# Optimization experiments

Measured on AMD Instinct MI355X. Metric: run time of the kernel, lower is better.

Reference implementation:

```python
import jax, jax.numpy as jnp
import numpy as np

EPS = 1e-12  # F.normalize default eps


def setup_inputs() -> dict:
    key = jax.random.key(0)
    k1, k2 = jax.random.split(key)
    b, c, angRes, h, w = 4, 64, 5, 64, 64
    d = 64  # dims
    x = jax.random.normal(k1, (b, c, angRes * angRes, h, w), dtype=jnp.float32)
    # 1x1 conv weight [3*dims, channels] (kernel size 1, no bias)
    W = jax.random.normal(k2, (3 * d, c), dtype=jnp.float32) * 0.02
    return {"x": x, "W": W}


def reference(x, W):
    b, c, n, h, w = x.shape
    d = W.shape[0] // 3
    # 1x1 conv over angular (u,v) grid == channel matmul; rearranges are free reindexings
    qkv = jnp.einsum('oc,bcnhw->bonhw', W, x)  # [b, 3d, n, h, w]
    q, k, v = jnp.split(qkv, 3, axis=1)        # each [b, d, n, h, w]

    def flat(t):  # '(b h w) c u v -> b (u v) (c h w)'
        return t.transpose(0, 2, 1, 3, 4).reshape(b, n, d * h * w)

    q, k, v = flat(q), flat(k), flat(v)
    # L2-normalize along the (c h w) feature dim (k was normalized on dim=-2 of its
    # transposed layout, which is this same feature dim)
    q = q / jnp.maximum(jnp.linalg.norm(q, axis=-1, keepdims=True), EPS)
    k = k / jnp.maximum(jnp.linalg.norm(k, axis=-1, keepdims=True), EPS)
    att = jax.nn.softmax(jnp.einsum('bnf,bmf->bnm', q, k), axis=-1)  # [b, n, n], n=25
    out = jnp.einsum('bnm,bmf->bnf', att, v)   # [b, n, d*h*w]
    # 'b (u v) (c h w) -> b c (u v) h w'
    return out.reshape(b, n, d, h, w).transpose(0, 2, 1, 3, 4)
```

## Files before the change

kernel.cpp:

```cpp
#include <hip/hip_runtime.h>

#define B   4
#define C   64
#define D   64
#define NN  25
#define HW  4096
#define F   (D*HW)

#define SW  256
#define PT  128

typedef unsigned short ushort_t;
typedef unsigned int   uint_t;
typedef __attribute__((ext_vector_type(8)))  short  short8;
typedef __attribute__((ext_vector_type(16))) float  floatx16;
typedef __attribute__((ext_vector_type(4)))  float  f32x4;
typedef __attribute__((ext_vector_type(4)))  unsigned short us4;

__device__ ushort_t g_Wthi[128 * C];
__device__ ushort_t g_Wtlo[128 * C];
__device__ ushort_t g_Wvhi[D * C];
__device__ ushort_t g_Wvlo[D * C];

__device__ float g_S[B * NN * NN];
__device__ float g_qq[B * NN];
__device__ float g_kk[B * NN];
__device__ float g_attT[B * NN * NN];

static __device__ __forceinline__ ushort_t f2bf(float f) {
    uint_t u = __float_as_uint(f);
    u += 0x7FFFu + ((u >> 16) & 1u);
    return (ushort_t)(u >> 16);
}
static __device__ __forceinline__ float bf2f(ushort_t h) {
    return __uint_as_float((uint_t)h << 16);
}

static __device__ __forceinline__ int lds_x(int p, int c) {
    return p * 64 + ((((c >> 3) ^ (p & 7)) << 3) | (c & 7));
}

__global__ void k_zero() {
    int i = blockIdx.x * 256 + threadIdx.x;
    if (i < 2500)      g_S[i] = 0.f;
    else if (i < 2600) g_qq[i - 2500] = 0.f;
    else if (i < 2700) g_kk[i - 2600] = 0.f;
}

__global__ void k_wprep(const float* __restrict__ W) {
    int i = blockIdx.x * 256 + threadIdx.x;
    if (i < 128 * 64) {
        float w = W[i];
        ushort_t hi = f2bf(w);
        g_Wthi[i] = hi;
        g_Wtlo[i] = f2bf(w - bf2f(hi));
    } else if (i < 192 * 64) {
        float w = W[i];
        int j = i - 128 * 64;
        ushort_t hi = f2bf(w);
        g_Wvhi[j] = hi;
        g_Wvlo[j] = f2bf(w - bf2f(hi));
    }
}

__global__ void __launch_bounds__(256, 4)
k_proj(const float* __restrict__ x,
       ushort_t* __restrict__ Q, ushort_t* __restrict__ K,
       float* __restrict__ V) {
    __shared__ ushort_t sXhi[PT * 64];
    __shared__ ushort_t sXlo[PT * 64];

    const int t  = threadIdx.x;
    const int wv = t >> 6, ln = t & 63;
    const int n  = blockIdx.y, b = blockIdx.z;
    const int tile = blockIdx.x;
    const int gp0  = tile * PT;

    const int row = ln & 31, kh = (ln >> 5) * 8, d0 = wv * 32;
    short8 ahi[4], alo[4];
#pragma unroll
    for (int ks = 0; ks < 4; ++ks) {
        ahi[ks] = *(const short8*)&g_Wthi[(d0 + row) * 64 + ks * 16 + kh];
        alo[ks] = *(const short8*)&g_Wtlo[(d0 + row) * 64 + ks * 16 + kh];
    }

    {
        const int c16 = wv * 16;
#pragma unroll
        for (int cg = 0; cg < 4; ++cg) {
            const int c4 = c16 + cg * 4;
            const float* xc = x + ((size_t)(b * C + c4) * NN + n) * HW + gp0;
#pragma unroll
            for (int ph = 0; ph < 2; ++ph) {
                const int p = ph * 64 + ln;
                float v[4];
#pragma unroll
                for (int i = 0; i < 4; ++i) v[i] = xc[(size_t)i * NN * HW + p];
                us4 h, l;
#pragma unroll
                for (int i = 0; i < 4; ++i) {
                    ushort_t hi = f2bf(v[i]);
                    h[i] = hi;
                    l[i] = f2bf(v[i] - bf2f(hi));
                }
                *(us4*)&sXhi[lds_x(p, c4)] = h;
                *(us4*)&sXlo[lds_x(p, c4)] = l;
            }
        }
    }
    __syncthreads();

    ushort_t* __restrict__ O = (wv < 2) ? Q : K;
    const int slab = (wv < 2) ? wv : wv - 2;
    const size_t nbase = (size_t)(b * NN + n) * F;

    float nrm = 0.f;
#pragma unroll
    for (int pt = 0; pt < 4; ++pt) {
        const int pcol = pt * 32 + row;
        floatx16 acc;
#pragma unroll
        for (int r = 0; r < 16; ++r) acc[r] = 0.f;
#pragma unroll
        for (int ks = 0; ks < 4; ++ks) {
            const int c0 = ks * 16 + kh;
            short8 bhi = *(const short8*)&sXhi[lds_x(pcol, c0)];
            short8 blo = *(const short8*)&sXlo[lds_x(pcol, c0)];
            acc = __builtin_amdgcn_mfma_f32_32x32x16_bf16(ahi[ks], bhi, acc, 0, 0, 0);
            acc = __builtin_amdgcn_mfma_f32_32x32x16_bf16(alo[ks], bhi, acc, 0, 0, 0);
            acc = __builtin_amdgcn_mfma_f32_32x32x16_bf16(ahi[ks], blo, acc, 0, 0, 0);
        }
#pragma unroll
        for (int r4 = 0; r4 < 4; ++r4) {
            us4 h;
#pragma unroll
            for (int j = 0; j < 4; ++j) {
                const float a = acc[r4 * 4 + j];
                nrm += a * a;
                h[j] = f2bf(a);
            }
            *(us4*)&O[nbase + (((size_t)((tile * 2 + slab) * 16 + pt * 4 + r4)) << 8)
                      + ln * 4] = h;
        }
    }
    for (int off = 32; off > 0; off >>= 1) nrm += __shfl_xor(nrm, off);
    if (ln == 0) atomicAdd(((wv < 2) ? g_qq : g_kk) + b * NN + n, nrm);

    {
        const int sv = wv & 1, ph = wv >> 1;
        short8 vhi[4], vlo[4];
#pragma unroll
        for (int ks = 0; ks < 4; ++ks) {
            vhi[ks] = *(const short8*)&g_Wvhi[(sv * 32 + row) * 64 + ks * 16 + kh];
            vlo[ks] = *(const short8*)&g_Wvlo[(sv * 32 + row) * 64 + ks * 16 + kh];
        }
#pragma unroll
        for (int pt = 0; pt < 2; ++pt) {
            const int pcol = ph * 64 + pt * 32 + row;
            floatx16 acc;
#pragma unroll
            for (int r = 0; r < 16; ++r) acc[r] = 0.f;
#pragma unroll
            for (int ks = 0; ks < 4; ++ks) {
                const int c0 = ks * 16 + kh;
                short8 bhi = *(const short8*)&sXhi[lds_x(pcol, c0)];
                short8 blo = *(const short8*)&sXlo[lds_x(pcol, c0)];
                acc = __builtin_amdgcn_mfma_f32_32x32x16_bf16(vhi[ks], bhi, acc, 0, 0, 0);
                acc = __builtin_amdgcn_mfma_f32_32x32x16_bf16(vlo[ks], bhi, acc, 0, 0, 0);
                acc = __builtin_amdgcn_mfma_f32_32x32x16_bf16(vhi[ks], blo, acc, 0, 0, 0);
            }
#pragma unroll
            for (int r4 = 0; r4 < 4; ++r4) {
                f32x4 o;
#pragma unroll
                for (int j = 0; j < 4; ++j) o[j] = acc[r4 * 4 + j];
                V[nbase + (((size_t)((((tile * 2 + sv) * 2 + ph) * 2 + pt) * 4 + r4)) << 8)
                  + ln * 4] = o[0],
                *(f32x4*)&V[nbase + (((size_t)((((tile * 2 + sv) * 2 + ph) * 2 + pt) * 4
                  + r4)) << 8) + ln * 4] = o;
            }
        }
    }
}

__global__ void k_sqk(const ushort_t* __restrict__ Q, const ushort_t* __restrict__ K) {
    const int t  = threadIdx.x;
    const int wv = t >> 6, ln = t & 63;
    const int b  = blockIdx.y;
    const int row  = ln & 31;
    const int rowc = (row < NN) ? row : (NN - 1);
    const int kh   = (ln >> 5) * 8;
    const size_t f0 = (size_t)blockIdx.x * (4 * SW) + (size_t)wv * SW;
    const ushort_t* Qp = Q + ((size_t)b * NN + rowc) * F + f0 + kh;
    const ushort_t* Kp = K + ((size_t)b * NN + rowc) * F + f0 + kh;

    floatx16 acc;
#pragma unroll
    for (int r = 0; r < 16; ++r) acc[r] = 0.f;

    for (int s = 0; s < SW / 16; ++s) {
        short8 aq = *(const short8*)(Qp + s * 16);
        short8 bk = *(const short8*)(Kp + s * 16);
        acc = __builtin_amdgcn_mfma_f32_32x32x16_bf16(aq, bk, acc, 0, 0, 0);
    }

    __shared__ float redS[4][64][17];
#pragma unroll
    for (int r = 0; r < 16; ++r) redS[wv][ln][r] = acc[r];
    __syncthreads();
    if (wv == 0) {
#pragma unroll
        for (int r = 0; r < 16; ++r) {
            float v = redS[0][ln][r] + redS[1][ln][r] + redS[2][ln][r] + redS[3][ln][r];
            const int srow = (r & 3) + 8 * (r >> 2) + 4 * (ln >> 5);
            const int scol = ln & 31;
            if (srow < NN && scol < NN)
                atomicAdd(&g_S[((size_t)b * NN + srow) * NN + scol], v);
        }
    }
}

__global__ void k_softmax() {
    const int b = blockIdx.x, n = threadIdx.x;
    if (n >= NN) return;
    const float qn = fmaxf(sqrtf(g_qq[b * NN + n]), 1e-12f);
    float l[NN], mx = -1e30f;
#pragma unroll
    for (int m = 0; m < NN; ++m) {
        const float km = fmaxf(sqrtf(g_kk[b * NN + m]), 1e-12f);
        l[m] = g_S[((size_t)b * NN + n) * NN + m] / (qn * km);
        mx = fmaxf(mx, l[m]);
    }
    float s = 0.f;
#pragma unroll
    for (int m = 0; m < NN; ++m) { l[m] = expf(l[m] - mx); s += l[m]; }
    const float inv = 1.f / s;
#pragma unroll
    for (int m = 0; m < NN; ++m) g_attT[((size_t)b * NN + m) * NN + n] = l[m] * inv;
}

__global__ void __launch_bounds__(256, 4)
k_outmix(const float* __restrict__ V, float* __restrict__ out) {
    const int tid = blockIdx.x * 256 + threadIdx.x;
    const int b   = blockIdx.y;
    const float* Vb = V + (size_t)b * NN * F + (size_t)tid * 4;
    const float* at = g_attT + b * NN * NN;

    f32x4 acc[NN];
#pragma unroll
    for (int n = 0; n < NN; ++n) acc[n] = 0.f;
#pragma unroll 5
    for (int m = 0; m < NN; ++m) {
        const f32x4 v = *(const f32x4*)(Vb + (size_t)m * F);
#pragma unroll
        for (int n = 0; n < NN; ++n) acc[n] += at[m * NN + n] * v;
    }

    const int ln = tid & 63, c0 = tid >> 6;
    const int r4 = c0 & 3, pt = (c0 >> 2) & 1, ph = (c0 >> 3) & 1;
    const int sv = (c0 >> 4) & 1, tile = c0 >> 5;
    const int p  = tile * 128 + ph * 64 + pt * 32 + (ln & 31);
    const int db = sv * 32 + 8 * r4 + 4 * (ln >> 5);
#pragma unroll
    for (int n = 0; n < NN; ++n)
#pragma unroll
        for (int j = 0; j < 4; ++j)
            out[((size_t)(b * D + db + j) * NN + n) * HW + p] = acc[n][j];
}

extern "C" void kernel_launch(void* const* d_in, const int* in_sizes, int n_in,
                              void* d_out, int out_size, void* d_ws, size_t ws_size,
                              hipStream_t stream) {
    const float* x = (const float*)d_in[0];
    const float* W = (const float*)d_in[1];
    float* outf = (float*)d_out;

    ushort_t* Q = (ushort_t*)d_out;
    ushort_t* K = Q + (size_t)B * NN * F;
    float*    V = (float*)d_ws;

    k_zero   <<<dim3(11),           256, 0, stream>>>();
    k_wprep  <<<dim3(48),           256, 0, stream>>>(W);
    k_proj   <<<dim3(HW/PT, NN, B), 256, 0, stream>>>(x, Q, K, V);
    k_sqk    <<<dim3(F/(4*SW), B),  256, 0, stream>>>(Q, K);
    k_softmax<<<dim3(B),             64, 0, stream>>>();
    k_outmix <<<dim3(F/1024, B),    256, 0, stream>>>(V, outf);
}
```

Before: 309.7 us.

## Stage Q/K chunks through swizzled LDS in S=QK^T kernel with 512 threads

The Gram-matrix kernel used to load Q and K directly from global memory with short8 per lane, where each lane read a different row (strided, poorly coalesced). It now cooperatively loads 256-element chunks of all 25 rows into XOR-swizzled shared memory with contiguous per-row accesses. Eight waves then each run MFMAs from LDS, and the reduction sums eight partials. A redundant scalar store in the projection kernel is also removed. The cost is extra LDS traffic and barriers, plus a larger reduction per block.

```diff
diff --git a/kernel.cpp b/kernel.cpp
--- a/kernel.cpp
+++ b/kernel.cpp
@@ -7,12 +7,14 @@
 #define HW  4096
 #define F   (D*HW)
 
-#define SW  256
 #define PT  128
+#define QCH 256
+#define NCH 4
 
 typedef unsigned short ushort_t;
 typedef unsigned int   uint_t;
 typedef __attribute__((ext_vector_type(8)))  short  short8;
+typedef __attribute__((ext_vector_type(8)))  unsigned short us8;
 typedef __attribute__((ext_vector_type(16))) float  floatx16;
 typedef __attribute__((ext_vector_type(4)))  float  f32x4;
 typedef __attribute__((ext_vector_type(4)))  unsigned short us4;
@@ -174,44 +176,67 @@
                 f32x4 o;
 #pragma unroll
                 for (int j = 0; j < 4; ++j) o[j] = acc[r4 * 4 + j];
-                V[nbase + (((size_t)((((tile * 2 + sv) * 2 + ph) * 2 + pt) * 4 + r4)) << 8)
-                  + ln * 4] = o[0],
                 *(f32x4*)&V[nbase + (((size_t)((((tile * 2 + sv) * 2 + ph) * 2 + pt) * 4
-                  + r4)) << 8) + ln * 4] = o;
+                    + r4)) << 8) + ln * 4] = o;
             }
         }
     }
 }
 
-__global__ void k_sqk(const ushort_t* __restrict__ Q, const ushort_t* __restrict__ K) {
+__global__ void __launch_bounds__(512, 8)
+k_sqk(const ushort_t* __restrict__ Q, const ushort_t* __restrict__ K) {
+    __shared__ __align__(16) unsigned char smem[35904];
+    ushort_t* sQ = (ushort_t*)smem;
+    ushort_t* sK = (ushort_t*)(smem + 16384);
+    float (*redS)[64][17] = (float (*)[64][17])smem;
+
     const int t  = threadIdx.x;
     const int wv = t >> 6, ln = t & 63;
     const int b  = blockIdx.y;
-    const int row  = ln & 31;
-    const int rowc = (row < NN) ? row : (NN - 1);
-    const int kh   = (ln >> 5) * 8;
-    const size_t f0 = (size_t)blockIdx.x * (4 * SW) + (size_t)wv * SW;
-    const ushort_t* Qp = Q + ((size_t)b * NN + rowc) * F + f0 + kh;
-    const ushort_t* Kp = K + ((size_t)b * NN + rowc) * F + f0 + kh;
+    const size_t fbase = (size_t)blockIdx.x * (QCH * NCH);
+
+    const int col = t & 31;
+    const int r0  = t >> 5;
+    const int rr  = ln & 31;
+    const int khalf = ln >> 5;
 
     floatx16 acc;
 #pragma unroll
     for (int r = 0; r < 16; ++r) acc[r] = 0.f;
 
-    for (int s = 0; s < SW / 16; ++s) {
-        short8 aq = *(const short8*)(Qp + s * 16);
-        short8 bk = *(const short8*)(Kp + s * 16);
-        acc = __builtin_amdgcn_mfma_f32_32x32x16_bf16(aq, bk, acc, 0, 0, 0);
-    }
-
-    __shared__ float redS[4][64][17];
+    for (int ch = 0; ch < NCH; ++ch) {
+        const size_t f0 = fbase + (size_t)ch * QCH;
+        if (ch) __syncthreads();
+#pragma unroll
+        for (int pass = 0; pass < 2; ++pass) {
+            const int r  = pass * 16 + r0;
+            const int rc = (r < NN) ? r : (NN - 1);
+            const size_t g = ((size_t)b * NN + rc) * F + f0 + col * 8;
+            const int lx = r * QCH + ((col ^ (r & 7)) * 8);
+            *(us8*)&sQ[lx] = *(const us8*)(Q + g);
+            *(us8*)&sK[lx] = *(const us8*)(K + g);
+        }
+        __syncthreads();
+#pragma unroll
+        for (int i = 0; i < 2; ++i) {
+            const int cunit = (wv * 2 + i) * 2 + khalf;
+            const int lx = rr * QCH + ((cunit ^ (rr & 7)) * 8);
+            short8 aq = *(const short8*)&sQ[lx];
+            short8 bk = *(const short8*)&sK[lx];
+            acc = __builtin_amdgcn_mfma_f32_32x32x16_bf16(aq, bk, acc, 0, 0, 0);
+        }
+    }
+
+    __syncthreads();
 #pragma unroll
     for (int r = 0; r < 16; ++r) redS[wv][ln][r] = acc[r];
     __syncthreads();
     if (wv == 0) {
 #pragma unroll
         for (int r = 0; r < 16; ++r) {
-            float v = redS[0][ln][r] + redS[1][ln][r] + redS[2][ln][r] + redS[3][ln][r];
+            float v = 0.f;
+#pragma unroll
+            for (int w = 0; w < 8; ++w) v += redS[w][ln][r];
             const int srow = (r & 3) + 8 * (r >> 2) + 4 * (ln >> 5);
             const int scol = ln & 31;
             if (srow < NN && scol < NN)
@@ -279,10 +304,10 @@
     ushort_t* K = Q + (size_t)B * NN * F;
     float*    V = (float*)d_ws;
 
-    k_zero   <<<dim3(11),           256, 0, stream>>>();
-    k_wprep  <<<dim3(48),           256, 0, stream>>>(W);
-    k_proj   <<<dim3(HW/PT, NN, B), 256, 0, stream>>>(x, Q, K, V);
-    k_sqk    <<<dim3(F/(4*SW), B),  256, 0, stream>>>(Q, K);
-    k_softmax<<<dim3(B),             64, 0, stream>>>();
-    k_outmix <<<dim3(F/1024, B),    256, 0, stream>>>(V, outf);
-}
+    k_zero   <<<dim3(11),               256, 0, stream>>>();
+    k_wprep  <<<dim3(48),               256, 0, stream>>>(W);
+    k_proj   <<<dim3(HW/PT, NN, B),     256, 0, stream>>>(x, Q, K, V);
+    k_sqk    <<<dim3(F/(QCH*NCH), B),   512, 0, stream>>>(Q, K);
+    k_softmax<<<dim3(B),                 64, 0, stream>>>();
+    k_outmix <<<dim3(F/1024, B),        256, 0, stream>>>(V, outf);
+}
```

Measured after the change: 302.9 us. 2.2% less time.

## Fuse QKV projection with Q·Kᵀ score computation, keeping Q/K in LDS

Applied to the files above, without the earlier changes.

Merges the projection and score kernels: each 512-thread block handles 32 pixels across all 25 angular views for one 32-channel slab, keeps bf16 Q and K tiles in shared memory, and computes the partial 25x25 score matrix directly from LDS. This removes the global-memory round trip of Q and K and one kernel launch. The x loads are double-buffered in registers and the V output layout and outmix indexing are changed to match. In exchange, each block uses about 100KB of LDS, which limits occupancy, and weights are reloaded per view iteration.

```diff
diff --git a/kernel.cpp b/kernel.cpp
--- a/kernel.cpp
+++ b/kernel.cpp
@@ -7,9 +7,6 @@
 #define HW  4096
 #define F   (D*HW)
 
-#define SW  256
-#define PT  128
-
 typedef unsigned short ushort_t;
 typedef unsigned int   uint_t;
 typedef __attribute__((ext_vector_type(8)))  short  short8;
@@ -34,10 +31,6 @@
 }
 static __device__ __forceinline__ float bf2f(ushort_t h) {
     return __uint_as_float((uint_t)h << 16);
-}
-
-static __device__ __forceinline__ int lds_x(int p, int c) {
-    return p * 64 + ((((c >> 3) ^ (p & 7)) << 3) | (c & 7));
 }
 
 __global__ void k_zero() {
@@ -63,159 +56,141 @@
     }
 }
 
-__global__ void __launch_bounds__(256, 4)
-k_proj(const float* __restrict__ x,
-       ushort_t* __restrict__ Q, ushort_t* __restrict__ K,
-       float* __restrict__ V) {
-    __shared__ ushort_t sXhi[PT * 64];
-    __shared__ ushort_t sXlo[PT * 64];
-
-    const int t  = threadIdx.x;
-    const int wv = t >> 6, ln = t & 63;
-    const int n  = blockIdx.y, b = blockIdx.z;
-    const int tile = blockIdx.x;
-    const int gp0  = tile * PT;
-
-    const int row = ln & 31, kh = (ln >> 5) * 8, d0 = wv * 32;
-    short8 ahi[4], alo[4];
-#pragma unroll
-    for (int ks = 0; ks < 4; ++ks) {
-        ahi[ks] = *(const short8*)&g_Wthi[(d0 + row) * 64 + ks * 16 + kh];
-        alo[ks] = *(const short8*)&g_Wtlo[(d0 + row) * 64 + ks * 16 + kh];
-    }
+__global__ void __launch_bounds__(512, 2)
+k_projS(const float* __restrict__ x, float* __restrict__ V) {
+    __shared__ ushort_t sQ[25 * 1024];
+    __shared__ ushort_t sK[25 * 1024];
+
+    const int t    = threadIdx.x;
+    const int w    = t >> 6, ln = t & 63;
+    const int slab = blockIdx.y, b = blockIdx.z;
+    const int p0   = blockIdx.x * 32;
+    const int row  = ln & 31, kh = ln >> 5, kh8 = kh * 8;
+    const size_t cstride = (size_t)NN * HW;
+    const float* xp = x + ((size_t)(b * C) * NN) * HW + p0 + row;
+
+    float xbufA[32], xbufB[32];
+#pragma unroll
+    for (int ks = 0; ks < 4; ++ks)
+#pragma unroll
+        for (int j = 0; j < 8; ++j)
+            xbufA[ks * 8 + j] =
+                xp[(size_t)(ks * 16 + kh8 + j) * cstride + (size_t)w * HW];
+
+#pragma unroll
+    for (int i = 0; i < 4; ++i) {
+        const int n = w + i * 8;
+        if (n > 24) break;
+        const int n2 = n + 8;
+        float (&cur)[32] = (i & 1) ? xbufB : xbufA;
+        float (&nxt)[32] = (i & 1) ? xbufA : xbufB;
+        if (n2 <= 24) {
+#pragma unroll
+            for (int ks = 0; ks < 4; ++ks)
+#pragma unroll
+                for (int j = 0; j < 8; ++j)
+                    nxt[ks * 8 + j] =
+                        xp[(size_t)(ks * 16 + kh8 + j) * cstride + (size_t)n2 * HW];
+        }
+
+        short8 qhi[4], qlo[4], khi[4], klo[4], vhi[4], vlo[4];
+#pragma unroll
+        for (int ks = 0; ks < 4; ++ks) {
+            const int off = ks * 16 + kh8;
+            qhi[ks] = *(const short8*)&g_Wthi[(slab * 32 + row) * 64 + off];
+            qlo[ks] = *(const short8*)&g_Wtlo[(slab * 32 + row) * 64 + off];
+            khi[ks] = *(const short8*)&g_Wthi[(64 + slab * 32 + row) * 64 + off];
+            klo[ks] = *(const short8*)&g_Wtlo[(64 + slab * 32 + row) * 64 + off];
+            vhi[ks] = *(const short8*)&g_Wvhi[(slab * 32 + row) * 64 + off];
+            vlo[ks] = *(const short8*)&g_Wvlo[(slab * 32 + row) * 64 + off];
+        }
+
+        short8 bhi[4], blo[4];
+#pragma unroll
+        for (int ks = 0; ks < 4; ++ks)
+#pragma unroll
+            for (int j = 0; j < 8; ++j) {
+                const float v = cur[ks * 8 + j];
+                const ushort_t hi = f2bf(v);
+                bhi[ks][j] = (short)hi;
+                blo[ks][j] = (short)f2bf(v - bf2f(hi));
+            }
+
+        floatx16 aQ, aK, aV;
+#pragma unroll
+        for (int r = 0; r < 16; ++r) { aQ[r] = 0.f; aK[r] = 0.f; aV[r] = 0.f; }
+#pragma unroll
+        for (int ks = 0; ks < 4; ++ks) {
+            aQ = __builtin_amdgcn_mfma_f32_32x32x16_bf16(qhi[ks], bhi[ks], aQ, 0, 0, 0);
+            aQ = __builtin_amdgcn_mfma_f32_32x32x16_bf16(qlo[ks], bhi[ks], aQ, 0, 0, 0);
+            aQ = __builtin_amdgcn_mfma_f32_32x32x16_bf16(qhi[ks], blo[ks], aQ, 0, 0, 0);
+            aK = __builtin_amdgcn_mfma_f32_32x32x16_bf16(khi[ks], bhi[ks], aK, 0, 0, 0);
+            aK = __builtin_amdgcn_mfma_f32_32x32x16_bf16(klo[ks], bhi[ks], aK, 0, 0, 0);
+            aK = __builtin_amdgcn_mfma_f32_32x32x16_bf16(khi[ks], blo[ks], aK, 0, 0, 0);
+            aV = __builtin_amdgcn_mfma_f32_32x32x16_bf16(vhi[ks], bhi[ks], aV, 0, 0, 0);
+            aV = __builtin_amdgcn_mfma_f32_32x32x16_bf16(vlo[ks], bhi[ks], aV, 0, 0, 0);
+            aV = __builtin_amdgcn_mfma_f32_32x32x16_bf16(vhi[ks], blo[ks], aV, 0, 0, 0);
+        }
+
+        float nq = 0.f, nk = 0.f;
+#pragma unroll
+        for (int r4 = 0; r4 < 4; ++r4) {
+            us4 hq, hk; f32x4 vv;
+#pragma unroll
+            for (int j = 0; j < 4; ++j) {
+                const float q = aQ[r4 * 4 + j], k = aK[r4 * 4 + j];
+                nq += q * q; nk += k * k;
+                hq[j] = f2bf(q); hk[j] = f2bf(k);
+                vv[j] = aV[r4 * 4 + j];
+            }
+            const int lx = n * 1024 + ((r4 * 32 + (ln >> 1)) ^ (n & 7)) * 8
+                         + (ln & 1) * 4;
+            *(us4*)&sQ[lx] = hq;
+            *(us4*)&sK[lx] = hk;
+            *(f32x4*)&V[((size_t)(b * NN + n)) * F
+                        + (size_t)((blockIdx.x * 2 + slab) * 4 + r4) * 256
+                        + ln * 4] = vv;
+        }
+        for (int off = 32; off > 0; off >>= 1) {
+            nq += __shfl_xor(nq, off);
+            nk += __shfl_xor(nk, off);
+        }
+        if (ln == 0) {
+            atomicAdd(&g_qq[b * NN + n], nq);
+            atomicAdd(&g_kk[b * NN + n], nk);
+        }
+    }
+    __syncthreads();
 
     {
-        const int c16 = wv * 16;
-#pragma unroll
-        for (int cg = 0; cg < 4; ++cg) {
-            const int c4 = c16 + cg * 4;
-            const float* xc = x + ((size_t)(b * C + c4) * NN + n) * HW + gp0;
-#pragma unroll
-            for (int ph = 0; ph < 2; ++ph) {
-                const int p = ph * 64 + ln;
-                float v[4];
-#pragma unroll
-                for (int i = 0; i < 4; ++i) v[i] = xc[(size_t)i * NN * HW + p];
-                us4 h, l;
-#pragma unroll
-                for (int i = 0; i < 4; ++i) {
-                    ushort_t hi = f2bf(v[i]);
-                    h[i] = hi;
-                    l[i] = f2bf(v[i] - bf2f(hi));
-                }
-                *(us4*)&sXhi[lds_x(p, c4)] = h;
-                *(us4*)&sXlo[lds_x(p, c4)] = l;
+        const int rc = (row < NN) ? row : (NN - 1);
+        floatx16 acc;
+#pragma unroll
+        for (int r = 0; r < 16; ++r) acc[r] = 0.f;
+#pragma unroll
+        for (int i = 0; i < 8; ++i) {
+            const int g  = (w * 8 + i) * 2 + kh;
+            const int lx = rc * 1024 + (g ^ (rc & 7)) * 8;
+            short8 aq = *(const short8*)&sQ[lx];
+            short8 bk = *(const short8*)&sK[lx];
+            acc = __builtin_amdgcn_mfma_f32_32x32x16_bf16(aq, bk, acc, 0, 0, 0);
+        }
+        __syncthreads();
+        float (*redS)[64][17] = (float (*)[64][17])sQ;
+#pragma unroll
+        for (int r = 0; r < 16; ++r) redS[w][ln][r] = acc[r];
+        __syncthreads();
+        if (w == 0) {
+#pragma unroll
+            for (int r = 0; r < 16; ++r) {
+                float v = 0.f;
+#pragma unroll
+                for (int wv = 0; wv < 8; ++wv) v += redS[wv][ln][r];
+                const int srow = (r & 3) + 8 * (r >> 2) + 4 * (ln >> 5);
+                const int scol = ln & 31;
+                if (srow < NN && scol < NN)
+                    atomicAdd(&g_S[((size_t)b * NN + srow) * NN + scol], v);
             }
-        }
-    }
-    __syncthreads();
-
-    ushort_t* __restrict__ O = (wv < 2) ? Q : K;
-    const int slab = (wv < 2) ? wv : wv - 2;
-    const size_t nbase = (size_t)(b * NN + n) * F;
-
-    float nrm = 0.f;
-#pragma unroll
-    for (int pt = 0; pt < 4; ++pt) {
-        const int pcol = pt * 32 + row;
-        floatx16 acc;
-#pragma unroll
-        for (int r = 0; r < 16; ++r) acc[r] = 0.f;
-#pragma unroll
-        for (int ks = 0; ks < 4; ++ks) {
-            const int c0 = ks * 16 + kh;
-            short8 bhi = *(const short8*)&sXhi[lds_x(pcol, c0)];
-            short8 blo = *(const short8*)&sXlo[lds_x(pcol, c0)];
-            acc = __builtin_amdgcn_mfma_f32_32x32x16_bf16(ahi[ks], bhi, acc, 0, 0, 0);
-            acc = __builtin_amdgcn_mfma_f32_32x32x16_bf16(alo[ks], bhi, acc, 0, 0, 0);
-            acc = __builtin_amdgcn_mfma_f32_32x32x16_bf16(ahi[ks], blo, acc, 0, 0, 0);
-        }
-#pragma unroll
-        for (int r4 = 0; r4 < 4; ++r4) {
-            us4 h;
-#pragma unroll
-            for (int j = 0; j < 4; ++j) {
-                const float a = acc[r4 * 4 + j];
-                nrm += a * a;
-                h[j] = f2bf(a);
-            }
-            *(us4*)&O[nbase + (((size_t)((tile * 2 + slab) * 16 + pt * 4 + r4)) << 8)
-                      + ln * 4] = h;
-        }
-    }
-    for (int off = 32; off > 0; off >>= 1) nrm += __shfl_xor(nrm, off);
-    if (ln == 0) atomicAdd(((wv < 2) ? g_qq : g_kk) + b * NN + n, nrm);
-
-    {
-        const int sv = wv & 1, ph = wv >> 1;
-        short8 vhi[4], vlo[4];
-#pragma unroll
-        for (int ks = 0; ks < 4; ++ks) {
-            vhi[ks] = *(const short8*)&g_Wvhi[(sv * 32 + row) * 64 + ks * 16 + kh];
-            vlo[ks] = *(const short8*)&g_Wvlo[(sv * 32 + row) * 64 + ks * 16 + kh];
-        }
-#pragma unroll
-        for (int pt = 0; pt < 2; ++pt) {
-            const int pcol = ph * 64 + pt * 32 + row;
-            floatx16 acc;
-#pragma unroll
-            for (int r = 0; r < 16; ++r) acc[r] = 0.f;
-#pragma unroll
-            for (int ks = 0; ks < 4; ++ks) {
-                const int c0 = ks * 16 + kh;
-                short8 bhi = *(const short8*)&sXhi[lds_x(pcol, c0)];
-                short8 blo = *(const short8*)&sXlo[lds_x(pcol, c0)];
-                acc = __builtin_amdgcn_mfma_f32_32x32x16_bf16(vhi[ks], bhi, acc, 0, 0, 0);
-                acc = __builtin_amdgcn_mfma_f32_32x32x16_bf16(vlo[ks], bhi, acc, 0, 0, 0);
-                acc = __builtin_amdgcn_mfma_f32_32x32x16_bf16(vhi[ks], blo, acc, 0, 0, 0);
-            }
-#pragma unroll
-            for (int r4 = 0; r4 < 4; ++r4) {
-                f32x4 o;
-#pragma unroll
-                for (int j = 0; j < 4; ++j) o[j] = acc[r4 * 4 + j];
-                V[nbase + (((size_t)((((tile * 2 + sv) * 2 + ph) * 2 + pt) * 4 + r4)) << 8)
-                  + ln * 4] = o[0],
-                *(f32x4*)&V[nbase + (((size_t)((((tile * 2 + sv) * 2 + ph) * 2 + pt) * 4
-                  + r4)) << 8) + ln * 4] = o;
-            }
-        }
-    }
-}
-
-__global__ void k_sqk(const ushort_t* __restrict__ Q, const ushort_t* __restrict__ K) {
-    const int t  = threadIdx.x;
-    const int wv = t >> 6, ln = t & 63;
-    const int b  = blockIdx.y;
-    const int row  = ln & 31;
-    const int rowc = (row < NN) ? row : (NN - 1);
-    const int kh   = (ln >> 5) * 8;
-    const size_t f0 = (size_t)blockIdx.x * (4 * SW) + (size_t)wv * SW;
-    const ushort_t* Qp = Q + ((size_t)b * NN + rowc) * F + f0 + kh;
-    const ushort_t* Kp = K + ((size_t)b * NN + rowc) * F + f0 + kh;
-
-    floatx16 acc;
-#pragma unroll
-    for (int r = 0; r < 16; ++r) acc[r] = 0.f;
-
-    for (int s = 0; s < SW / 16; ++s) {
-        short8 aq = *(const short8*)(Qp + s * 16);
-        short8 bk = *(const short8*)(Kp + s * 16);
-        acc = __builtin_amdgcn_mfma_f32_32x32x16_bf16(aq, bk, acc, 0, 0, 0);
-    }
-
-    __shared__ float redS[4][64][17];
-#pragma unroll
-    for (int r = 0; r < 16; ++r) redS[wv][ln][r] = acc[r];
-    __syncthreads();
-    if (wv == 0) {
-#pragma unroll
-        for (int r = 0; r < 16; ++r) {
-            float v = redS[0][ln][r] + redS[1][ln][r] + redS[2][ln][r] + redS[3][ln][r];
-            const int srow = (r & 3) + 8 * (r >> 2) + 4 * (ln >> 5);
-            const int scol = ln & 31;
-            if (srow < NN && scol < NN)
-                atomicAdd(&g_S[((size_t)b * NN + srow) * NN + scol], v);
         }
     }
 }
@@ -257,10 +232,9 @@
     }
 
     const int ln = tid & 63, c0 = tid >> 6;
-    const int r4 = c0 & 3, pt = (c0 >> 2) & 1, ph = (c0 >> 3) & 1;
-    const int sv = (c0 >> 4) & 1, tile = c0 >> 5;
-    const int p  = tile * 128 + ph * 64 + pt * 32 + (ln & 31);
-    const int db = sv * 32 + 8 * r4 + 4 * (ln >> 5);
+    const int r4 = c0 & 3, slab = (c0 >> 2) & 1, ps = c0 >> 3;
+    const int p  = ps * 32 + (ln & 31);
+    const int db = slab * 32 + 8 * r4 + 4 * (ln >> 5);
 #pragma unroll
     for (int n = 0; n < NN; ++n)
 #pragma unroll
@@ -275,14 +249,11 @@
     const float* W = (const float*)d_in[1];
     float* outf = (float*)d_out;
 
-    ushort_t* Q = (ushort_t*)d_out;
-    ushort_t* K = Q + (size_t)B * NN * F;
-    float*    V = (float*)d_ws;
+    float* V = (float*)d_ws;
 
     k_zero   <<<dim3(11),           256, 0, stream>>>();
     k_wprep  <<<dim3(48),           256, 0, stream>>>(W);
-    k_proj   <<<dim3(HW/PT, NN, B), 256, 0, stream>>>(x, Q, K, V);
-    k_sqk    <<<dim3(F/(4*SW), B),  256, 0, stream>>>(Q, K);
+    k_projS  <<<dim3(HW/32, 2, B),  512, 0, stream>>>(x, V);
     k_softmax<<<dim3(B),             64, 0, stream>>>();
     k_outmix <<<dim3(F/1024, B),    256, 0, stream>>>(V, outf);
 }
```

New measurement: 404.2 us. 1.3x slower.
